# Performance work log

Measured on AMD Instinct MI355X. Metric: run time of the kernel, lower is better.

## Reference

```python
import jax, jax.numpy as jnp
import numpy as np

N, D, E, H, TOP_K = 16384, 1024, 8, 2048, 2


def setup_inputs() -> dict:
    key = jax.random.key(0)
    ks = jax.random.split(key, 5)
    sd_d = 1.0 / np.sqrt(D)
    sd_h = 1.0 / np.sqrt(H)
    return {
        "x": jax.random.normal(ks[0], (N, D), dtype=jnp.float32),
        "Wg": jax.random.normal(ks[1], (D, E), dtype=jnp.float32) * sd_d,
        "bg": jnp.zeros((E,), jnp.float32),
        "W1": jax.random.normal(ks[2], (E, D, H), dtype=jnp.float32) * sd_d,
        "b1": jnp.zeros((E, H), jnp.float32),
        "W2": jax.random.normal(ks[3], (E, H, D), dtype=jnp.float32) * sd_h,
        "b2": jnp.zeros((E, D), jnp.float32),
    }


def reference(x, Wg, bg, W1, b1, W2, b2):
    # Gating: softmax over experts, then top-k with renormalized weights.
    gate_logits = x @ Wg + bg                      # [N, E]
    gate_probs = jax.nn.softmax(gate_logits, axis=-1)
    topk_p, topk_i = jax.lax.top_k(gate_probs, TOP_K)   # [N, K]
    topk_p = topk_p / topk_p.sum(axis=-1, keepdims=True)
    # Dense all-expert MLP (faithful to reference: every expert on every token).
    # Dropout(0.1) is inference-mode identity.
    h = jax.nn.gelu(jnp.einsum('nd,edh->neh', x, W1) + b1, approximate=False)  # [N, E, H]
    y = jnp.einsum('neh,ehd->ned', h, W2) + b2     # [N, E, D]
    # Gather selected experts and combine with routing weights; residual add.
    sel = jnp.take_along_axis(y, topk_i[:, :, None], axis=1)  # [N, K, D]
    out = jnp.sum(topk_p[:, :, None] * sel, axis=1) + x       # [N, D]
    return out
```

## Files before the change

### kernel.cpp

```cpp
#include <hip/hip_runtime.h>
#include <hip/hip_bf16.h>
#include <cstdint>
#include <cstddef>


#define N_TOK 16384
#define DIM   1024
#define NEXP  8
#define HID   2048
#define CAP   (2*N_TOK + NEXP*128)
#define CHUNK_TILES 66
#define CHUNK_ROWS  (CHUNK_TILES*128)
#define NCHUNK 4

typedef short  bf16x8 __attribute__((ext_vector_type(8)));
typedef float  f32x4  __attribute__((ext_vector_type(4)));

__device__ __forceinline__ unsigned short f2bf(float f) {
  union { float f; unsigned u; } v; v.f = f;
  unsigned r = v.u + 0x7fffu + ((v.u >> 16) & 1u);
  return (unsigned short)(r >> 16);
}

#define GLOAD_LDS16(gp, lp)                                                    \
  __builtin_amdgcn_global_load_lds(                                            \
      (const __attribute__((address_space(1))) void*)(gp),                     \
      (__attribute__((address_space(3))) void*)(lp), 16, 0, 0)

__global__ void convert_x_kernel(const float* __restrict__ x,
                                 unsigned short* __restrict__ xb,
                                 float* __restrict__ out) {
  size_t i = (size_t)blockIdx.x * 256 + threadIdx.x;
  float4 v = ((const float4*)x)[i];
  ((float4*)out)[i] = v;
  ushort4 o;
  o.x = f2bf(v.x); o.y = f2bf(v.y); o.z = f2bf(v.z); o.w = f2bf(v.w);
  ((ushort4*)xb)[i] = o;
}

__global__ void transpose_kernel(const float* __restrict__ src,
                                 unsigned short* __restrict__ dst,
                                 int R, int C) {
  __shared__ float tile[32][33];
  int e = blockIdx.z;
  int rb = blockIdx.y * 32, cb = blockIdx.x * 32;
  int tx = threadIdx.x & 31, ty = threadIdx.x >> 5;
  const float* s = src + ((size_t)e * R + rb) * C + cb;
#pragma unroll
  for (int i = 0; i < 4; ++i)
    tile[ty + i*8][tx] = s[(size_t)(ty + i*8) * C + tx];
  __syncthreads();
  unsigned short* d = dst + ((size_t)e * C + cb) * R + rb;
#pragma unroll
  for (int i = 0; i < 4; ++i) {
    int r2 = ty + i*8;
    d[(size_t)r2 * R + tx] = f2bf(tile[tx][r2]);
  }
}

__global__ void gating_kernel(const float* __restrict__ x,
                              const float* __restrict__ Wg,
                              const float* __restrict__ bg,
                              int* __restrict__ tok_ids,
                              float* __restrict__ tok_w) {
  int wid  = threadIdx.x >> 6;
  int lane = threadIdx.x & 63;
  int t = blockIdx.x * 4 + wid;
  const float* xr = x + (size_t)t * DIM;
  float acc[NEXP];
#pragma unroll
  for (int e = 0; e < NEXP; ++e) acc[e] = 0.f;
#pragma unroll
  for (int i = 0; i < 4; ++i) {
    int d0 = i * 256 + lane * 4;
    float4 xv = *(const float4*)(xr + d0);
    const float* wr = Wg + (size_t)d0 * NEXP;
#pragma unroll
    for (int j = 0; j < 4; ++j) {
      float xs = (j == 0) ? xv.x : (j == 1) ? xv.y : (j == 2) ? xv.z : xv.w;
      float4 wa = *(const float4*)(wr + j * NEXP);
      float4 wb = *(const float4*)(wr + j * NEXP + 4);
      acc[0] += xs * wa.x; acc[1] += xs * wa.y; acc[2] += xs * wa.z; acc[3] += xs * wa.w;
      acc[4] += xs * wb.x; acc[5] += xs * wb.y; acc[6] += xs * wb.z; acc[7] += xs * wb.w;
    }
  }
#pragma unroll
  for (int off = 32; off >= 1; off >>= 1)
#pragma unroll
    for (int e = 0; e < NEXP; ++e)
      acc[e] += __shfl_xor(acc[e], off, 64);
  if (lane == 0) {
#pragma unroll
    for (int e = 0; e < NEXP; ++e) acc[e] += bg[e];
    float m = acc[0];
#pragma unroll
    for (int e = 1; e < NEXP; ++e) m = fmaxf(m, acc[e]);
    float p[NEXP];
#pragma unroll
    for (int e = 0; e < NEXP; ++e) p[e] = expf(acc[e] - m);
    int i0 = 0; float v0 = p[0];
#pragma unroll
    for (int e = 1; e < NEXP; ++e) if (p[e] > v0) { v0 = p[e]; i0 = e; }
    int i1 = -1; float v1 = -1.f;
#pragma unroll
    for (int e = 0; e < NEXP; ++e) if (e != i0 && p[e] > v1) { v1 = p[e]; i1 = e; }
    float s = v0 + v1;
    tok_ids[t*2]     = i0;  tok_ids[t*2 + 1] = i1;
    tok_w[t*2]       = v0 / s;  tok_w[t*2 + 1] = v1 / s;
  }
}

__global__ void hist_kernel(const int* __restrict__ tok_ids, int* __restrict__ meta) {
  __shared__ int red[256];
  int e = blockIdx.x;
  int c = 0;
  for (int i = threadIdx.x; i < 2 * N_TOK; i += 256) c += (tok_ids[i] == e) ? 1 : 0;
  red[threadIdx.x] = c;
  __syncthreads();
  for (int s = 128; s > 0; s >>= 1) {
    if (threadIdx.x < s) red[threadIdx.x] += red[threadIdx.x + s];
    __syncthreads();
  }
  if (threadIdx.x == 0) meta[e] = red[0];
}

__global__ void offsets_kernel(int* meta) {
  if (threadIdx.x == 0 && blockIdx.x == 0) {
    int off = 0;
    for (int e = 0; e < NEXP; ++e) {
      meta[8 + e]  = off;
      meta[17 + e] = off;
      off += (meta[e] + 127) & ~127;
    }
    meta[16] = off;
  }
}

__global__ void filldef_kernel(int* __restrict__ list_token, float* __restrict__ list_w) {
  int i = blockIdx.x * 256 + threadIdx.x;
  if (i < CAP) { list_token[i] = 0; list_w[i] = 0.f; }
}

__global__ void scatter_kernel(const int* __restrict__ tok_ids,
                               const float* __restrict__ tok_w,
                               int* __restrict__ meta,
                               int* __restrict__ list_token,
                               float* __restrict__ list_w) {
  int idx  = blockIdx.x * 256 + threadIdx.x;
  int lane = threadIdx.x & 63;
  int e = tok_ids[idx];
  float w = tok_w[idx];
  int pos = 0;
#pragma unroll 1
  for (int ee = 0; ee < NEXP; ++ee) {
    bool mine = (e == ee);
    unsigned long long mask = __ballot(mine);
    if (mask) {
      int leader = __ffsll((unsigned long long)mask) - 1;
      int cnt = (int)__popcll(mask);
      int base = 0;
      if (lane == leader) base = atomicAdd(&meta[17 + ee], cnt);
      base = __shfl(base, leader, 64);
      if (mine) pos = base + (int)__popcll(mask & ((1ull << lane) - 1ull));
    }
  }
  list_token[pos] = idx >> 1;
  list_w[pos]     = w;
}


__global__ void gemm1_kernel(const unsigned short* __restrict__ xb,
                             const unsigned short* __restrict__ w1t,
                             const float* __restrict__ b1,
                             const int* __restrict__ meta,
                             const int* __restrict__ list_token,
                             unsigned short* __restrict__ hb,
                             int chunk_base) {
  const int tid = threadIdx.x, lane = tid & 63;
  const int wid = tid >> 6, wr = wid >> 1, wc = wid & 1;
  const int bx = blockIdx.x, by = blockIdx.y;
  const int r0 = chunk_base + by * 128;
  const int* offs = meta + 8;
  if (r0 >= offs[8]) return;
  int e = 0;
#pragma unroll
  for (int k = 1; k < NEXP; ++k) if (r0 >= offs[k]) e = k;

  __shared__ __align__(16) unsigned short As[128 * 64];
  __shared__ __align__(16) unsigned short Bs[128 * 64];

  f32x4 acc[4][4] = {};

  const unsigned short* bsrc = w1t + ((size_t)e * HID + (size_t)bx * 128) * DIM;
  int lrow[4], lk0[4];
  const unsigned short* arow[4];
#pragma unroll
  for (int i = 0; i < 4; ++i) {
    int g = i * 256 + tid;
    int row = g >> 3, u = g & 7;
    lrow[i] = row;
    lk0[i]  = ((u ^ (row & 7)) << 3);
    arow[i] = xb + (size_t)list_token[r0 + row] * DIM;
  }
  const int llo = lane & 15, lhi = lane >> 4;

  for (int kt = 0; kt < DIM / 64; ++kt) {
    __syncthreads();
#pragma unroll
    for (int i = 0; i < 4; ++i) {
      int g4 = (i * 256 + (tid & ~63)) * 8;
      GLOAD_LDS16(arow[i] + kt * 64 + lk0[i], &As[g4]);
      GLOAD_LDS16(bsrc + (size_t)lrow[i] * DIM + kt * 64 + lk0[i], &Bs[g4]);
    }
    __syncthreads();
    bf16x8 af[4][2], bfr[4][2];
#pragma unroll
    for (int m = 0; m < 4; ++m)
#pragma unroll
      for (int kk = 0; kk < 2; ++kk) {
        int ra = wr * 64 + m * 16 + llo;
        af[m][kk]  = *(const bf16x8*)&As[(ra * 64 + kk * 32 + lhi * 8) ^ ((llo & 7) << 3)];
        int rb = wc * 64 + m * 16 + llo;
        bfr[m][kk] = *(const bf16x8*)&Bs[(rb * 64 + kk * 32 + lhi * 8) ^ ((llo & 7) << 3)];
      }
#pragma unroll
    for (int kk = 0; kk < 2; ++kk)
#pragma unroll
      for (int m = 0; m < 4; ++m)
#pragma unroll
        for (int n = 0; n < 4; ++n)
          acc[m][n] = __builtin_amdgcn_mfma_f32_16x16x32_bf16(af[m][kk], bfr[n][kk], acc[m][n], 0, 0, 0);
  }

  const float* b1e = b1 + (size_t)e * HID + bx * 128;
#pragma unroll
  for (int m = 0; m < 4; ++m)
#pragma unroll
    for (int n = 0; n < 4; ++n)
#pragma unroll
      for (int j = 0; j < 4; ++j) {
        int rl = wr * 64 + m * 16 + lhi * 4 + j;
        int cl = wc * 64 + n * 16 + llo;
        float v = acc[m][n][j] + b1e[cl];
        v = 0.5f * v * (1.0f + erff(v * 0.70710678118f));
        hb[(size_t)(by * 128 + rl) * HID + bx * 128 + cl] = f2bf(v);
      }
}

__global__ void gemm2_kernel(const unsigned short* __restrict__ hb,
                             const unsigned short* __restrict__ w2t,
                             const float* __restrict__ b2,
                             const int* __restrict__ meta,
                             const int* __restrict__ list_token,
                             const float* __restrict__ list_w,
                             float* __restrict__ out,
                             int chunk_base) {
  const int tid = threadIdx.x, lane = tid & 63;
  const int wid = tid >> 6, wr = wid >> 1, wc = wid & 1;
  const int bx = blockIdx.x, by = blockIdx.y;
  const int r0 = chunk_base + by * 128;
  const int* offs = meta + 8;
  if (r0 >= offs[8]) return;
  int e = 0;
#pragma unroll
  for (int k = 1; k < NEXP; ++k) if (r0 >= offs[k]) e = k;

  __shared__ __align__(16) unsigned short As[128 * 64];
  __shared__ __align__(16) unsigned short Bs[128 * 64];

  f32x4 acc[4][4] = {};

  const unsigned short* bsrc = w2t + ((size_t)e * DIM + (size_t)bx * 128) * HID;
  int lrow[4], lk0[4];
  const unsigned short* arow[4];
#pragma unroll
  for (int i = 0; i < 4; ++i) {
    int g = i * 256 + tid;
    int row = g >> 3, u = g & 7;
    lrow[i] = row;
    lk0[i]  = ((u ^ (row & 7)) << 3);
    arow[i] = hb + (size_t)(by * 128 + row) * HID;
  }
  const int llo = lane & 15, lhi = lane >> 4;

  for (int kt = 0; kt < HID / 64; ++kt) {
    __syncthreads();
#pragma unroll
    for (int i = 0; i < 4; ++i) {
      int g4 = (i * 256 + (tid & ~63)) * 8;
      GLOAD_LDS16(arow[i] + kt * 64 + lk0[i], &As[g4]);
      GLOAD_LDS16(bsrc + (size_t)lrow[i] * HID + kt * 64 + lk0[i], &Bs[g4]);
    }
    __syncthreads();
    bf16x8 af[4][2], bfr[4][2];
#pragma unroll
    for (int m = 0; m < 4; ++m)
#pragma unroll
      for (int kk = 0; kk < 2; ++kk) {
        int ra = wr * 64 + m * 16 + llo;
        af[m][kk]  = *(const bf16x8*)&As[(ra * 64 + kk * 32 + lhi * 8) ^ ((llo & 7) << 3)];
        int rb = wc * 64 + m * 16 + llo;
        bfr[m][kk] = *(const bf16x8*)&Bs[(rb * 64 + kk * 32 + lhi * 8) ^ ((llo & 7) << 3)];
      }
#pragma unroll
    for (int kk = 0; kk < 2; ++kk)
#pragma unroll
      for (int m = 0; m < 4; ++m)
#pragma unroll
        for (int n = 0; n < 4; ++n)
          acc[m][n] = __builtin_amdgcn_mfma_f32_16x16x32_bf16(af[m][kk], bfr[n][kk], acc[m][n], 0, 0, 0);
  }

  const float* b2e = b2 + (size_t)e * DIM + bx * 128;
#pragma unroll
  for (int m = 0; m < 4; ++m)
#pragma unroll
    for (int n = 0; n < 4; ++n)
#pragma unroll
      for (int j = 0; j < 4; ++j) {
        int rl = wr * 64 + m * 16 + lhi * 4 + j;
        int cl = wc * 64 + n * 16 + llo;
        int rg = r0 + rl;
        float v = acc[m][n][j] + b2e[cl];
        float w = list_w[rg];
        atomicAdd(&out[(size_t)list_token[rg] * DIM + bx * 128 + cl], w * v);
      }
}

extern "C" void kernel_launch(void* const* d_in, const int* in_sizes, int n_in,
                              void* d_out, int out_size, void* d_ws, size_t ws_size,
                              hipStream_t stream) {
  const float* x  = (const float*)d_in[0];
  const float* Wg = (const float*)d_in[1];
  const float* bg = (const float*)d_in[2];
  const float* W1 = (const float*)d_in[3];
  const float* b1 = (const float*)d_in[4];
  const float* W2 = (const float*)d_in[5];
  const float* b2 = (const float*)d_in[6];
  float* out = (float*)d_out;

  char* ws = (char*)d_ws;
  size_t off = 0;
  auto alloc = [&](size_t bytes) -> void* {
    void* p = ws + off;
    off = (off + bytes + 255) & ~(size_t)255;
    return p;
  };
  unsigned short* xb   = (unsigned short*)alloc((size_t)N_TOK * DIM * 2);
  unsigned short* w1t  = (unsigned short*)alloc((size_t)NEXP * HID * DIM * 2);
  unsigned short* w2t  = (unsigned short*)alloc((size_t)NEXP * DIM * HID * 2);
  unsigned short* hb   = (unsigned short*)alloc((size_t)CHUNK_ROWS * HID * 2);
  int*   tok_ids    = (int*)alloc((size_t)N_TOK * 2 * 4);
  float* tok_w      = (float*)alloc((size_t)N_TOK * 2 * 4);
  int*   list_token = (int*)alloc((size_t)CAP * 4);
  float* list_w     = (float*)alloc((size_t)CAP * 4);
  int*   meta       = (int*)alloc(256);

  convert_x_kernel<<<(N_TOK * DIM / 4) / 256, 256, 0, stream>>>(x, xb, out);
  transpose_kernel<<<dim3(HID / 32, DIM / 32, NEXP), 256, 0, stream>>>(W1, w1t, DIM, HID);
  transpose_kernel<<<dim3(DIM / 32, HID / 32, NEXP), 256, 0, stream>>>(W2, w2t, HID, DIM);

  gating_kernel<<<N_TOK / 4, 256, 0, stream>>>(x, Wg, bg, tok_ids, tok_w);
  hist_kernel<<<NEXP, 256, 0, stream>>>(tok_ids, meta);
  offsets_kernel<<<1, 64, 0, stream>>>(meta);
  filldef_kernel<<<(CAP + 255) / 256, 256, 0, stream>>>(list_token, list_w);
  scatter_kernel<<<(2 * N_TOK) / 256, 256, 0, stream>>>(tok_ids, tok_w, meta, list_token, list_w);

  for (int c = 0; c < NCHUNK; ++c) {
    gemm1_kernel<<<dim3(HID / 128, CHUNK_TILES), 256, 0, stream>>>(
        xb, w1t, b1, meta, list_token, hb, c * CHUNK_ROWS);
    gemm2_kernel<<<dim3(DIM / 128, CHUNK_TILES), 256, 0, stream>>>(
        hb, w2t, b2, meta, list_token, list_w, out, c * CHUNK_ROWS);
  }
}
```

Before: 965.3 us.

## Fuse x conversion into gating, add XCD-aware tile swizzle, fewer GEMM chunks

Folds the x-to-bf16 conversion and residual copy into the gating kernel, so x is read only once. Replaces the 2D GEMM grid with a 1D grid remapped so that consecutive tiles land on the same XCD, which should improve L2 reuse of expert weights and activation rows. It also sizes the intermediate buffer from the available workspace, dropping to a single chunk when it fits, which cuts kernel launches and idle tail tiles. The risk is that the chunk count now depends on workspace size, and the swizzle assumes 8 XCDs.

```diff
diff --git a/kernel.cpp b/kernel.cpp
--- a/kernel.cpp
+++ b/kernel.cpp
@@ -9,9 +9,7 @@
 #define NEXP  8
 #define HID   2048
 #define CAP   (2*N_TOK + NEXP*128)
-#define CHUNK_TILES 66
-#define CHUNK_ROWS  (CHUNK_TILES*128)
-#define NCHUNK 4
+#define TOT_TILES (CAP/128)
 
 typedef short  bf16x8 __attribute__((ext_vector_type(8)));
 typedef float  f32x4  __attribute__((ext_vector_type(4)));
@@ -26,17 +24,6 @@
   __builtin_amdgcn_global_load_lds(                                            \
       (const __attribute__((address_space(1))) void*)(gp),                     \
       (__attribute__((address_space(3))) void*)(lp), 16, 0, 0)
-
-__global__ void convert_x_kernel(const float* __restrict__ x,
-                                 unsigned short* __restrict__ xb,
-                                 float* __restrict__ out) {
-  size_t i = (size_t)blockIdx.x * 256 + threadIdx.x;
-  float4 v = ((const float4*)x)[i];
-  ((float4*)out)[i] = v;
-  ushort4 o;
-  o.x = f2bf(v.x); o.y = f2bf(v.y); o.z = f2bf(v.z); o.w = f2bf(v.w);
-  ((ushort4*)xb)[i] = o;
-}
 
 __global__ void transpose_kernel(const float* __restrict__ src,
                                  unsigned short* __restrict__ dst,
@@ -61,12 +48,16 @@
 __global__ void gating_kernel(const float* __restrict__ x,
                               const float* __restrict__ Wg,
                               const float* __restrict__ bg,
+                              unsigned short* __restrict__ xb,
+                              float* __restrict__ out,
                               int* __restrict__ tok_ids,
                               float* __restrict__ tok_w) {
   int wid  = threadIdx.x >> 6;
   int lane = threadIdx.x & 63;
   int t = blockIdx.x * 4 + wid;
   const float* xr = x + (size_t)t * DIM;
+  float4* outr = (float4*)(out + (size_t)t * DIM);
+  ushort4* xbr = (ushort4*)(xb + (size_t)t * DIM);
   float acc[NEXP];
 #pragma unroll
   for (int e = 0; e < NEXP; ++e) acc[e] = 0.f;
@@ -74,6 +65,10 @@
   for (int i = 0; i < 4; ++i) {
     int d0 = i * 256 + lane * 4;
     float4 xv = *(const float4*)(xr + d0);
+    outr[i * 64 + lane] = xv;
+    ushort4 o;
+    o.x = f2bf(xv.x); o.y = f2bf(xv.y); o.z = f2bf(xv.z); o.w = f2bf(xv.w);
+    xbr[i * 64 + lane] = o;
     const float* wr = Wg + (size_t)d0 * NEXP;
 #pragma unroll
     for (int j = 0; j < 4; ++j) {
@@ -169,17 +164,29 @@
 }
 
 
+__device__ __forceinline__ void xcd_swizzle(int nx_log2, int base_tile,
+                                            int& bx, int& by) {
+  int nwg = gridDim.x;
+  int wgid = blockIdx.x;
+  int q = nwg >> 3, r = nwg & 7;
+  int xcd = wgid & 7, loc = wgid >> 3;
+  int swz = (xcd < r ? xcd * (q + 1) : r * (q + 1) + (xcd - r) * q) + loc;
+  bx = swz & ((1 << nx_log2) - 1);
+  by = base_tile + (swz >> nx_log2);
+}
+
 __global__ void gemm1_kernel(const unsigned short* __restrict__ xb,
                              const unsigned short* __restrict__ w1t,
                              const float* __restrict__ b1,
                              const int* __restrict__ meta,
                              const int* __restrict__ list_token,
                              unsigned short* __restrict__ hb,
-                             int chunk_base) {
+                             int base_tile) {
   const int tid = threadIdx.x, lane = tid & 63;
   const int wid = tid >> 6, wr = wid >> 1, wc = wid & 1;
-  const int bx = blockIdx.x, by = blockIdx.y;
-  const int r0 = chunk_base + by * 128;
+  int bx, by;
+  xcd_swizzle(4, base_tile, bx, by);
+  const int r0 = by * 128;
   const int* offs = meta + 8;
   if (r0 >= offs[8]) return;
   int e = 0;
@@ -243,7 +250,7 @@
         int cl = wc * 64 + n * 16 + llo;
         float v = acc[m][n][j] + b1e[cl];
         v = 0.5f * v * (1.0f + erff(v * 0.70710678118f));
-        hb[(size_t)(by * 128 + rl) * HID + bx * 128 + cl] = f2bf(v);
+        hb[(size_t)((by - base_tile) * 128 + rl) * HID + bx * 128 + cl] = f2bf(v);
       }
 }
 
@@ -254,11 +261,12 @@
                              const int* __restrict__ list_token,
                              const float* __restrict__ list_w,
                              float* __restrict__ out,
-                             int chunk_base) {
+                             int base_tile) {
   const int tid = threadIdx.x, lane = tid & 63;
   const int wid = tid >> 6, wr = wid >> 1, wc = wid & 1;
-  const int bx = blockIdx.x, by = blockIdx.y;
-  const int r0 = chunk_base + by * 128;
+  int bx, by;
+  xcd_swizzle(3, base_tile, bx, by);
+  const int r0 = by * 128;
   const int* offs = meta + 8;
   if (r0 >= offs[8]) return;
   int e = 0;
@@ -279,7 +287,7 @@
     int row = g >> 3, u = g & 7;
     lrow[i] = row;
     lk0[i]  = ((u ^ (row & 7)) << 3);
-    arow[i] = hb + (size_t)(by * 128 + row) * HID;
+    arow[i] = hb + (size_t)((by - base_tile) * 128 + row) * HID;
   }
   const int llo = lane & 15, lhi = lane >> 4;
 
@@ -349,27 +357,33 @@
   unsigned short* xb   = (unsigned short*)alloc((size_t)N_TOK * DIM * 2);
   unsigned short* w1t  = (unsigned short*)alloc((size_t)NEXP * HID * DIM * 2);
   unsigned short* w2t  = (unsigned short*)alloc((size_t)NEXP * DIM * HID * 2);
-  unsigned short* hb   = (unsigned short*)alloc((size_t)CHUNK_ROWS * HID * 2);
   int*   tok_ids    = (int*)alloc((size_t)N_TOK * 2 * 4);
   float* tok_w      = (float*)alloc((size_t)N_TOK * 2 * 4);
   int*   list_token = (int*)alloc((size_t)CAP * 4);
   float* list_w     = (float*)alloc((size_t)CAP * 4);
   int*   meta       = (int*)alloc(256);
 
-  convert_x_kernel<<<(N_TOK * DIM / 4) / 256, 256, 0, stream>>>(x, xb, out);
+  size_t hb_full = (size_t)CAP * HID * 2;
+  int nchunk = 4;
+  if (ws_size - off >= hb_full + 4096)           nchunk = 1;
+  else if (ws_size - off >= hb_full / 2 + 4096)  nchunk = 2;
+  int tiles_per_chunk = TOT_TILES / nchunk;
+  unsigned short* hb = (unsigned short*)alloc(hb_full / nchunk);
+
+  gating_kernel<<<N_TOK / 4, 256, 0, stream>>>(x, Wg, bg, xb, out, tok_ids, tok_w);
+
   transpose_kernel<<<dim3(HID / 32, DIM / 32, NEXP), 256, 0, stream>>>(W1, w1t, DIM, HID);
   transpose_kernel<<<dim3(DIM / 32, HID / 32, NEXP), 256, 0, stream>>>(W2, w2t, HID, DIM);
 
-  gating_kernel<<<N_TOK / 4, 256, 0, stream>>>(x, Wg, bg, tok_ids, tok_w);
   hist_kernel<<<NEXP, 256, 0, stream>>>(tok_ids, meta);
   offsets_kernel<<<1, 64, 0, stream>>>(meta);
   filldef_kernel<<<(CAP + 255) / 256, 256, 0, stream>>>(list_token, list_w);
   scatter_kernel<<<(2 * N_TOK) / 256, 256, 0, stream>>>(tok_ids, tok_w, meta, list_token, list_w);
 
-  for (int c = 0; c < NCHUNK; ++c) {
-    gemm1_kernel<<<dim3(HID / 128, CHUNK_TILES), 256, 0, stream>>>(
-        xb, w1t, b1, meta, list_token, hb, c * CHUNK_ROWS);
-    gemm2_kernel<<<dim3(DIM / 128, CHUNK_TILES), 256, 0, stream>>>(
-        hb, w2t, b2, meta, list_token, list_w, out, c * CHUNK_ROWS);
-  }
-}
+  for (int c = 0; c < nchunk; ++c) {
+    gemm1_kernel<<<16 * tiles_per_chunk, 256, 0, stream>>>(
+        xb, w1t, b1, meta, list_token, hb, c * tiles_per_chunk);
+    gemm2_kernel<<<8 * tiles_per_chunk, 256, 0, stream>>>(
+        hb, w2t, b2, meta, list_token, list_w, out, c * tiles_per_chunk);
+  }
+}
```

After: 774.8 us. 1.25x faster.
